# Optimization experiments

Hardware: AMD Instinct MI355X
Metric: run time of the kernel (lower is better)

Reference implementation:

```python
import jax, jax.numpy as jnp
import numpy as np

N_ROWS = 100000   # sparse matrix rows (nodes)
N_COLS = 8192     # input feature dim
UNITS = 128
NNZ = 2000000     # ~20 nonzeros per row


def setup_inputs() -> dict:
    key = jax.random.key(0)
    k1, k2, k3, k4, k5 = jax.random.split(key, 5)
    vals = jax.random.normal(k1, (NNZ,), dtype=jnp.float32)
    rows = jax.random.randint(k2, (NNZ,), 0, N_ROWS, dtype=jnp.int32)
    cols = jax.random.randint(k3, (NNZ,), 0, N_COLS, dtype=jnp.int32)
    # GlorotUniform-style scale for W, matching the TF initializer statistics
    limit = jnp.sqrt(6.0 / (N_COLS + UNITS)).astype(jnp.float32)
    W = jax.random.uniform(k4, (N_COLS, UNITS), dtype=jnp.float32, minval=-limit, maxval=limit)
    b = jax.random.uniform(k5, (UNITS,), dtype=jnp.float32, minval=-limit, maxval=limit)
    return {"vals": vals, "rows": rows, "cols": cols, "W": W, "b": b, "num_rows": N_ROWS}


def reference(vals, rows, cols, W, b, num_rows):
    # sparse (COO) [num_rows, F] @ dense W [F, units]:
    # gather the W row for each nonzero, scale by the nonzero value,
    # then scatter-add into the output row -> segment_sum over `rows`.
    gathered = W[cols] * vals[:, None]            # [nnz, units]
    out = jax.ops.segment_sum(gathered, rows, num_segments=num_rows)  # [num_rows, units]
    return out + b                                 # bias add (use_bias=True)
```

## Files before the change

### kernel.cpp

```cpp
#include <hip/hip_runtime.h>
#include <hip/hip_fp16.h>


#define UNITS 128
#define SCAN_BLK 1024
#define BROW 98
#define CBROW 784
#define NCC 128
#define CCAP 17664
#define CH3 2048
#define SLOTS 40
#define OVF_CAP 256
#define SPILL_CAP 8192


__global__ __launch_bounds__(512, 8) void partition_kernel(
        const float* __restrict__ vals, const int* __restrict__ rows,
        const int* __restrict__ cols, const float* __restrict__ W,
        __half2* __restrict__ Wh, int* __restrict__ ccur,
        float2* __restrict__ sortedA, float2* __restrict__ spill,
        int nnz, int nbcc, int wn2) {
    __shared__ float2 sStage[CH3];
    __shared__ unsigned short sBkt[CH3];
    __shared__ int hist[NCC];
    __shared__ int gdelta[NCC];

    const int t = threadIdx.x;
    const int lane = t & 63;
    const int w = t >> 6;
    const int bb = blockIdx.x;

    {
        const float2* W2 = (const float2*)W;
        int stride = gridDim.x * 512;
        for (int i = bb * 512 + t; i < wn2; i += stride)
            Wh[i] = __float22half2_rn(W2[i]);
    }

    const int chunk0 = bb * CH3;
    int n = nnz - chunk0;
    if (n > CH3) n = CH3;

    if (t < NCC) hist[t] = 0;
    __syncthreads();

    int rbuf[4];
#pragma unroll
    for (int j = 0; j < 4; ++j) {
        int r = j * 512 + t;
        int rv = -1;
        if (r < n) {
            rv = rows[chunk0 + r];
            atomicAdd(&hist[rv / CBROW], 1);
        }
        rbuf[j] = rv;
    }
    __syncthreads();

    if (w == 0) {
        int a0 = hist[2 * lane], a1 = hist[2 * lane + 1];
        int ps = a0 + a1;
        int inc = ps;
#pragma unroll
        for (int o = 1; o < 64; o <<= 1) {
            int u = __shfl_up(inc, o);
            if (lane >= o) inc += u;
        }
        int excl = inc - ps;
        int s0 = 2 * lane, s1 = 2 * lane + 1;
        int g0 = (s0 < nbcc && a0 > 0) ? atomicAdd(&ccur[s0 * 16], a0) : 0;
        int g1 = (s1 < nbcc && a1 > 0) ? atomicAdd(&ccur[s1 * 16], a1) : 0;
        gdelta[s0] = s0 * CCAP + g0 - excl;
        gdelta[s1] = s1 * CCAP + g1 - (excl + a0);
        hist[s0] = excl;
        hist[s1] = excl + a0;
    }
    __syncthreads();

#pragma unroll
    for (int j = 0; j < 4; ++j) {
        int rv = rbuf[j];
        if (rv >= 0) {
            int r = j * 512 + t;
            int bkt = rv / CBROW;
            int rlo = rv - bkt * CBROW;
            int pos = atomicAdd(&hist[bkt], 1);
            float v = vals[chunk0 + r];
            int col = cols[chunk0 + r];
            sStage[pos] = make_float2(v, __int_as_float(col | (rlo << 13)));
            sBkt[pos] = (unsigned short)bkt;
        }
    }
    __syncthreads();

    int* spill_cnt = &ccur[NCC * 16];
    for (int s = t; s < n; s += 512) {
        float2 e = sStage[s];
        int bkt = sBkt[s];
        int dest = gdelta[bkt] + s;
        if (dest < (bkt + 1) * CCAP) {
            sortedA[dest] = e;
        } else {
            int sp = atomicAdd(spill_cnt, 1);
            if (sp < SPILL_CAP) {
                int pk = __float_as_int(e.y);
                int row = bkt * CBROW + (pk >> 13);
                spill[sp] = make_float2(e.x, __int_as_float((pk & 8191) | (row << 13)));
            }
        }
    }
}


__global__ __launch_bounds__(512, 8) void fused_sort_compute_kernel(
        const float2* __restrict__ A, const int* __restrict__ ccur,
        const __half2* __restrict__ Wh, const float* __restrict__ b,
        float* __restrict__ out, const float2* __restrict__ spill, int NR) {
    __shared__ float2 st[BROW * SLOTS];
    __shared__ float2 ovf[OVF_CAP];
    __shared__ int cnt_s[BROW + 6];
    __shared__ int ovf_n;
    __shared__ int spill_n;
    const int t = threadIdx.x;
    const int lane = t & 63;
    const int w = t >> 6;

    const int nwg = gridDim.x;
    const int orig = blockIdx.x;
    const int q = nwg >> 3, r8 = nwg & 7, xcd = orig & 7, idx = orig >> 3;
    const int f = (xcd < r8 ? xcd * (q + 1) : r8 * (q + 1) + (xcd - r8) * q) + idx;

    const int c = f >> 3, sb = f & 7;
    const int r0 = f * BROW;
    const int rlo0 = sb * BROW;
    const size_t base = (size_t)c * CCAP;
    int segn = ccur[c * 16];
    if (segn > CCAP) segn = CCAP;

    const float2 bias = ((const float2*)b)[lane];

    if (t < BROW + 6) cnt_s[t] = 0;
    if (t == 0) {
        ovf_n = 0;
        int sn = ccur[NCC * 16];
        spill_n = (sn > SPILL_CAP) ? SPILL_CAP : sn;
    }
    for (int i = t; i < BROW * SLOTS; i += 512)
        st[i] = make_float2(0.f, __int_as_float(0));
    __syncthreads();

    const float4* A4 = (const float4*)(A + base);
    const int seg2 = segn >> 1;
    for (int k2 = t; k2 < seg2; k2 += 512) {
        float4 qv = A4[k2];
        {
            int pk = __float_as_int(qv.y);
            unsigned rl = (unsigned)(pk >> 13) - rlo0;
            if (rl < BROW) {
                int p = atomicAdd(&cnt_s[rl], 1);
                if (p < SLOTS) st[rl * SLOTS + p] = make_float2(qv.x, __int_as_float(pk & 8191));
                else {
                    int qn = atomicAdd(&ovf_n, 1);
                    if (qn < OVF_CAP) ovf[qn] = make_float2(qv.x, __int_as_float((pk & 8191) | (rl << 13)));
                }
            }
        }
        {
            int pk = __float_as_int(qv.w);
            unsigned rl = (unsigned)(pk >> 13) - rlo0;
            if (rl < BROW) {
                int p = atomicAdd(&cnt_s[rl], 1);
                if (p < SLOTS) st[rl * SLOTS + p] = make_float2(qv.z, __int_as_float(pk & 8191));
                else {
                    int qn = atomicAdd(&ovf_n, 1);
                    if (qn < OVF_CAP) ovf[qn] = make_float2(qv.z, __int_as_float((pk & 8191) | (rl << 13)));
                }
            }
        }
    }
    if ((segn & 1) && t == 0) {
        float2 e = A[base + segn - 1];
        int pk = __float_as_int(e.y);
        unsigned rl = (unsigned)(pk >> 13) - rlo0;
        if (rl < BROW) {
            int p = atomicAdd(&cnt_s[rl], 1);
            if (p < SLOTS) st[rl * SLOTS + p] = make_float2(e.x, __int_as_float(pk & 8191));
            else {
                int qn = atomicAdd(&ovf_n, 1);
                if (qn < OVF_CAP) ovf[qn] = make_float2(e.x, __int_as_float((pk & 8191) | (rl << 13)));
            }
        }
    }
    __syncthreads();

    const int on = (ovf_n > OVF_CAP) ? OVF_CAP : ovf_n;
    const int sn = spill_n;
    for (int rA = w; rA < BROW; rA += 16) {
        const int rB = rA + 8;
        const bool hasB = (rB < BROW);
        int cA = cnt_s[rA]; if (cA > SLOTS) cA = SLOTS; cA = (cA + 3) & ~3;
        int cB = 0;
        if (hasB) { cB = cnt_s[rB]; if (cB > SLOTS) cB = SLOTS; cB = (cB + 3) & ~3; }
        const float2* sA = &st[rA * SLOTS];
        const float2* sB = &st[(hasB ? rB : rA) * SLOTS];
        const int m = (cA > cB) ? cA : cB;
        float axA0 = 0.f, ayA0 = 0.f, axA1 = 0.f, ayA1 = 0.f;
        float axB0 = 0.f, ayB0 = 0.f, axB1 = 0.f, ayB1 = 0.f;
        for (int k = 0; k < m; k += 4) {
            if (k < cA) {
                float2 p0 = sA[k], p1 = sA[k + 1], p2 = sA[k + 2], p3 = sA[k + 3];
                int c0 = __float_as_int(p0.y) & 8191;
                int c1 = __float_as_int(p1.y) & 8191;
                int c2 = __float_as_int(p2.y) & 8191;
                int c3 = __float_as_int(p3.y) & 8191;
                float2 w0 = __half22float2(Wh[c0 * 64 + lane]);
                float2 w1 = __half22float2(Wh[c1 * 64 + lane]);
                float2 w2 = __half22float2(Wh[c2 * 64 + lane]);
                float2 w3 = __half22float2(Wh[c3 * 64 + lane]);
                axA0 += p0.x * w0.x; ayA0 += p0.x * w0.y;
                axA1 += p1.x * w1.x; ayA1 += p1.x * w1.y;
                axA0 += p2.x * w2.x; ayA0 += p2.x * w2.y;
                axA1 += p3.x * w3.x; ayA1 += p3.x * w3.y;
            }
            if (k < cB) {
                float2 p0 = sB[k], p1 = sB[k + 1], p2 = sB[k + 2], p3 = sB[k + 3];
                int c0 = __float_as_int(p0.y) & 8191;
                int c1 = __float_as_int(p1.y) & 8191;
                int c2 = __float_as_int(p2.y) & 8191;
                int c3 = __float_as_int(p3.y) & 8191;
                float2 w0 = __half22float2(Wh[c0 * 64 + lane]);
                float2 w1 = __half22float2(Wh[c1 * 64 + lane]);
                float2 w2 = __half22float2(Wh[c2 * 64 + lane]);
                float2 w3 = __half22float2(Wh[c3 * 64 + lane]);
                axB0 += p0.x * w0.x; ayB0 += p0.x * w0.y;
                axB1 += p1.x * w1.x; ayB1 += p1.x * w1.y;
                axB0 += p2.x * w2.x; ayB0 += p2.x * w2.y;
                axB1 += p3.x * w3.x; ayB1 += p3.x * w3.y;
            }
        }
        {
            int grow = r0 + rA;
            if (grow < NR) {
                for (int q2 = 0; q2 < on; ++q2) {
                    float2 eo = ovf[q2];
                    int pk = __float_as_int(eo.y);
                    if ((pk >> 13) == rA) {
                        float2 wv = __half22float2(Wh[(pk & 8191) * 64 + lane]);
                        axA0 += eo.x * wv.x; ayA0 += eo.x * wv.y;
                    }
                }
                for (int s2 = 0; s2 < sn; ++s2) {
                    float2 es = spill[s2];
                    int pk = __float_as_int(es.y);
                    if ((pk >> 13) == grow) {
                        float2 wv = __half22float2(Wh[(pk & 8191) * 64 + lane]);
                        axA0 += es.x * wv.x; ayA0 += es.x * wv.y;
                    }
                }
                ((float2*)out)[(size_t)grow * 64 + lane] =
                    make_float2(axA0 + axA1 + bias.x, ayA0 + ayA1 + bias.y);
            }
        }
        if (hasB) {
            int grow = r0 + rB;
            if (grow < NR) {
                for (int q2 = 0; q2 < on; ++q2) {
                    float2 eo = ovf[q2];
                    int pk = __float_as_int(eo.y);
                    if ((pk >> 13) == rB) {
                        float2 wv = __half22float2(Wh[(pk & 8191) * 64 + lane]);
                        axB0 += eo.x * wv.x; ayB0 += eo.x * wv.y;
                    }
                }
                for (int s2 = 0; s2 < sn; ++s2) {
                    float2 es = spill[s2];
                    int pk = __float_as_int(es.y);
                    if ((pk >> 13) == grow) {
                        float2 wv = __half22float2(Wh[(pk & 8191) * 64 + lane]);
                        axB0 += es.x * wv.x; ayB0 += es.x * wv.y;
                    }
                }
                ((float2*)out)[(size_t)grow * 64 + lane] =
                    make_float2(axB0 + axB1 + bias.x, ayB0 + ayB1 + bias.y);
            }
        }
    }
}


__global__ void hist_kernel(const int* __restrict__ rows, int* __restrict__ counts, int nnz) {
    int i = blockIdx.x * blockDim.x + threadIdx.x;
    if (i < nnz) atomicAdd(&counts[rows[i]], 1);
}

__global__ void scan1_kernel(const int* __restrict__ counts, int* __restrict__ tmp,
                             int* __restrict__ bsums, int NR, int NS) {
    __shared__ int s[SCAN_BLK];
    int t = threadIdx.x;
    int i = blockIdx.x * SCAN_BLK + t;
    int x = (i < NR) ? counts[i] : 0;
    s[t] = x;
    __syncthreads();
    for (int off = 1; off < SCAN_BLK; off <<= 1) {
        int v = (t >= off) ? s[t - off] : 0;
        __syncthreads();
        s[t] += v;
        __syncthreads();
    }
    if (i < NS) tmp[i] = s[t] - x;
    if (t == SCAN_BLK - 1) bsums[blockIdx.x] = s[SCAN_BLK - 1];
}

__global__ void scan2_kernel(int* __restrict__ bsums, int nb) {
    if (threadIdx.x == 0 && blockIdx.x == 0) {
        int run = 0;
        for (int i = 0; i < nb; ++i) { int c = bsums[i]; bsums[i] = run; run += c; }
    }
}

__global__ void scan3_kernel(const int* __restrict__ tmp, const int* __restrict__ bsums,
                             int* __restrict__ row_start, int* __restrict__ cursor,
                             int NR, int NS) {
    int i = blockIdx.x * blockDim.x + threadIdx.x;
    if (i < NS) {
        int v = tmp[i] + bsums[i >> 10];
        row_start[i] = v;
        if (i < NR) cursor[i] = v;
    }
}

__global__ void scatter_sort_kernel(const float* __restrict__ vals, const int* __restrict__ rows,
                                    const int* __restrict__ cols, int* __restrict__ cursor,
                                    float2* __restrict__ sorted, int nnz) {
    int i = blockIdx.x * blockDim.x + threadIdx.x;
    if (i < nnz) {
        int r = rows[i];
        int p = atomicAdd(&cursor[r], 1);
        sorted[p] = make_float2(vals[i], __int_as_float(cols[i]));
    }
}

__global__ void compute_kernel(const float2* __restrict__ sorted, const int* __restrict__ row_start,
                               const float* __restrict__ W, const float* __restrict__ b,
                               float* __restrict__ out, int NR) {
    int lane = threadIdx.x & 63;
    int wv = threadIdx.x >> 6;
    int row = blockIdx.x * 4 + wv;
    if (row >= NR) return;
    int start = row_start[row];
    int end   = row_start[row + 1];
    const float2* W2 = (const float2*)W;
    float accx0 = 0.f, accy0 = 0.f, accx1 = 0.f, accy1 = 0.f;
    for (int base = start; base < end; base += 64) {
        int m = end - base;
        if (m > 64) m = 64;
        float2 p = make_float2(0.f, __int_as_float(0));
        if (lane < m) p = sorted[base + lane];
        int vi = __float_as_int(p.x);
        int ci = __float_as_int(p.y);
        int rounds = (m + 3) & ~3;
        for (int j = 0; j < rounds; j += 4) {
            float v0 = __int_as_float(__builtin_amdgcn_readlane(vi, j));
            int   c0 = __builtin_amdgcn_readlane(ci, j);
            float v1 = __int_as_float(__builtin_amdgcn_readlane(vi, j + 1));
            int   c1 = __builtin_amdgcn_readlane(ci, j + 1);
            float v2 = __int_as_float(__builtin_amdgcn_readlane(vi, j + 2));
            int   c2 = __builtin_amdgcn_readlane(ci, j + 2);
            float v3 = __int_as_float(__builtin_amdgcn_readlane(vi, j + 3));
            int   c3 = __builtin_amdgcn_readlane(ci, j + 3);
            float2 w0 = W2[c0 * 64 + lane];
            float2 w1 = W2[c1 * 64 + lane];
            float2 w2 = W2[c2 * 64 + lane];
            float2 w3 = W2[c3 * 64 + lane];
            accx0 += v0 * w0.x; accy0 += v0 * w0.y;
            accx1 += v1 * w1.x; accy1 += v1 * w1.y;
            accx0 += v2 * w2.x; accy0 += v2 * w2.y;
            accx1 += v3 * w3.x; accy1 += v3 * w3.y;
        }
    }
    float2 bb = ((const float2*)b)[lane];
    ((float2*)out)[(size_t)row * 64 + lane] =
        make_float2(accx0 + accx1 + bb.x, accy0 + accy1 + bb.y);
}


__global__ void init_bias_kernel(float* __restrict__ out, const float* __restrict__ b, int total4) {
    const float4* b4 = (const float4*)b;
    float4* out4 = (float4*)out;
    int stride = gridDim.x * blockDim.x;
    for (int j = blockIdx.x * blockDim.x + threadIdx.x; j < total4; j += stride)
        out4[j] = b4[j & 31];
}

__global__ void scatter_atomic_kernel(const float* __restrict__ vals, const int* __restrict__ rows,
                                      const int* __restrict__ cols, const float* __restrict__ W,
                                      float* __restrict__ out, int nnz) {
    long long idx = (long long)blockIdx.x * blockDim.x + threadIdx.x;
    int i = (int)(idx >> 5);
    int c = (int)(idx & 31);
    if (i >= nnz) return;
    int row = rows[i], col = cols[i];
    float v = vals[i];
    float4 w = ((const float4*)W)[col * 32 + c];
    float* o = out + (size_t)row * UNITS + (c << 2);
    atomicAdd(o + 0, v * w.x);
    atomicAdd(o + 1, v * w.y);
    atomicAdd(o + 2, v * w.z);
    atomicAdd(o + 3, v * w.w);
}

extern "C" void kernel_launch(void* const* d_in, const int* in_sizes, int n_in,
                              void* d_out, int out_size, void* d_ws, size_t ws_size,
                              hipStream_t stream) {
    const float* vals = (const float*)d_in[0];
    const int*   rows = (const int*)d_in[1];
    const int*   cols = (const int*)d_in[2];
    const float* W    = (const float*)d_in[3];
    const float* b    = (const float*)d_in[4];
    float* out = (float*)d_out;

    const int nnz = in_sizes[0];
    const int NW  = in_sizes[3];
    const int NR  = out_size / UNITS;
    const int NS  = NR + 1;
    const int NB  = (NS + SCAN_BLK - 1) / SCAN_BLK;
    const int nbf  = (NR + BROW - 1) / BROW;
    const int nbcc = (NR + CBROW - 1) / CBROW;

    auto align = [](size_t x) { return (x + 255) & ~(size_t)255; };

    size_t off_ccur    = 0;
    size_t off_wh      = align(off_ccur + (size_t)(NCC * 16 + 1) * 4);
    size_t off_sortedA = align(off_wh + (size_t)NW * 2);
    size_t off_spill   = align(off_sortedA + (size_t)NCC * CCAP * 8);
    size_t needed_full = off_spill + (size_t)SPILL_CAP * 8;

    size_t t2_counts   = 0;
    size_t t2_tmp      = align(t2_counts + (size_t)NR * 4);
    size_t t2_bsums    = align(t2_tmp    + (size_t)NS * 4);
    size_t t2_rowstart = align(t2_bsums  + (size_t)NB * 4);
    size_t t2_cursor   = align(t2_rowstart + (size_t)NS * 4);
    size_t t2_sorted   = align(t2_cursor + (size_t)NR * 4);
    size_t needed_r2   = t2_sorted + (size_t)nnz * 8;

    char* ws = (char*)d_ws;

    if (ws_size >= needed_full && nbcc >= 1 && nbcc <= NCC && NR >= 1) {
        int*     ccur    = (int*)(ws + off_ccur);
        __half2* Wh      = (__half2*)(ws + off_wh);
        float2*  sortedA = (float2*)(ws + off_sortedA);
        float2*  spill   = (float2*)(ws + off_spill);

        hipMemsetAsync(ccur, 0, (size_t)(NCC * 16 + 1) * 4, stream);
        {
            int grid = (nnz + CH3 - 1) / CH3;
            partition_kernel<<<grid, 512, 0, stream>>>(vals, rows, cols, W, Wh,
                                                       ccur, sortedA, spill,
                                                       nnz, nbcc, NW / 2);
        }
        fused_sort_compute_kernel<<<nbf, 512, 0, stream>>>(sortedA, ccur, Wh, b,
                                                           out, spill, NR);
    } else if (ws_size >= needed_r2) {
        int*    counts    = (int*)(ws + t2_counts);
        int*    tmp       = (int*)(ws + t2_tmp);
        int*    bsums     = (int*)(ws + t2_bsums);
        int*    row_start = (int*)(ws + t2_rowstart);
        int*    cursor    = (int*)(ws + t2_cursor);
        float2* sorted    = (float2*)(ws + t2_sorted);

        hipMemsetAsync(counts, 0, (size_t)NR * 4, stream);
        {
            int block = 256, grid = (nnz + block - 1) / block;
            hist_kernel<<<grid, block, 0, stream>>>(rows, counts, nnz);
        }
        scan1_kernel<<<NB, SCAN_BLK, 0, stream>>>(counts, tmp, bsums, NR, NS);
        scan2_kernel<<<1, 64, 0, stream>>>(bsums, NB);
        {
            int block = 256, grid = (NS + block - 1) / block;
            scan3_kernel<<<grid, block, 0, stream>>>(tmp, bsums, row_start, cursor, NR, NS);
        }
        {
            int block = 256, grid = (nnz + block - 1) / block;
            scatter_sort_kernel<<<grid, block, 0, stream>>>(vals, rows, cols, cursor, sorted, nnz);
        }
        {
            int grid = (NR + 3) / 4;
            compute_kernel<<<grid, 256, 0, stream>>>(sorted, row_start, W, b, out, NR);
        }
    } else {
        int total4 = out_size / 4;
        int block = 256;
        int grid = (total4 + block - 1) / block;
        init_bias_kernel<<<grid, block, 0, stream>>>(out, b, total4);
        long long total_threads = (long long)nnz * 32;
        long long g2 = (total_threads + block - 1) / block;
        scatter_atomic_kernel<<<(int)g2, block, 0, stream>>>(vals, rows, cols, W, out, nnz);
    }
}
```

Baseline: 169.8 us.

## Double partition chunk size and make the gather-accumulate loop branchless

Each partition block now handles 4096 nonzeros instead of 2048. The bucket index array shrinks to bytes so LDS use grows less, and the per-thread row buffer doubles. This means fewer blocks, fewer global cursor atomics and fewer scattered writes. In the compute kernel, the two rows processed by a wave are now loaded and accumulated together without per-row branches, padded to the larger of the two counts. This trades extra, possibly wasted, slot reads for more independent W gathers in flight. It relies on unused slots holding zero values and raises LDS use per partition block, which may lower occupancy.

```diff
diff --git a/kernel.cpp b/kernel.cpp
--- a/kernel.cpp
+++ b/kernel.cpp
@@ -8,7 +8,7 @@
 #define CBROW 784
 #define NCC 128
 #define CCAP 17664
-#define CH3 2048
+#define CH3 4096
 #define SLOTS 40
 #define OVF_CAP 256
 #define SPILL_CAP 8192
@@ -21,7 +21,7 @@
         float2* __restrict__ sortedA, float2* __restrict__ spill,
         int nnz, int nbcc, int wn2) {
     __shared__ float2 sStage[CH3];
-    __shared__ unsigned short sBkt[CH3];
+    __shared__ unsigned char sBkt[CH3];
     __shared__ int hist[NCC];
     __shared__ int gdelta[NCC];
 
@@ -44,9 +44,9 @@
     if (t < NCC) hist[t] = 0;
     __syncthreads();
 
-    int rbuf[4];
+    int rbuf[8];
 #pragma unroll
-    for (int j = 0; j < 4; ++j) {
+    for (int j = 0; j < 8; ++j) {
         int r = j * 512 + t;
         int rv = -1;
         if (r < n) {
@@ -78,7 +78,7 @@
     __syncthreads();
 
 #pragma unroll
-    for (int j = 0; j < 4; ++j) {
+    for (int j = 0; j < 8; ++j) {
         int rv = rbuf[j];
         if (rv >= 0) {
             int r = j * 512 + t;
@@ -88,7 +88,7 @@
             float v = vals[chunk0 + r];
             int col = cols[chunk0 + r];
             sStage[pos] = make_float2(v, __int_as_float(col | (rlo << 13)));
-            sBkt[pos] = (unsigned short)bkt;
+            sBkt[pos] = (unsigned char)bkt;
         }
     }
     __syncthreads();
@@ -198,45 +198,42 @@
     for (int rA = w; rA < BROW; rA += 16) {
         const int rB = rA + 8;
         const bool hasB = (rB < BROW);
-        int cA = cnt_s[rA]; if (cA > SLOTS) cA = SLOTS; cA = (cA + 3) & ~3;
+        int cA = cnt_s[rA]; if (cA > SLOTS) cA = SLOTS;
         int cB = 0;
-        if (hasB) { cB = cnt_s[rB]; if (cB > SLOTS) cB = SLOTS; cB = (cB + 3) & ~3; }
+        if (hasB) { cB = cnt_s[rB]; if (cB > SLOTS) cB = SLOTS; }
         const float2* sA = &st[rA * SLOTS];
         const float2* sB = &st[(hasB ? rB : rA) * SLOTS];
-        const int m = (cA > cB) ? cA : cB;
+        int m = (cA > cB) ? cA : cB;
+        m = (m + 3) & ~3;
         float axA0 = 0.f, ayA0 = 0.f, axA1 = 0.f, ayA1 = 0.f;
         float axB0 = 0.f, ayB0 = 0.f, axB1 = 0.f, ayB1 = 0.f;
         for (int k = 0; k < m; k += 4) {
-            if (k < cA) {
-                float2 p0 = sA[k], p1 = sA[k + 1], p2 = sA[k + 2], p3 = sA[k + 3];
-                int c0 = __float_as_int(p0.y) & 8191;
-                int c1 = __float_as_int(p1.y) & 8191;
-                int c2 = __float_as_int(p2.y) & 8191;
-                int c3 = __float_as_int(p3.y) & 8191;
-                float2 w0 = __half22float2(Wh[c0 * 64 + lane]);
-                float2 w1 = __half22float2(Wh[c1 * 64 + lane]);
-                float2 w2 = __half22float2(Wh[c2 * 64 + lane]);
-                float2 w3 = __half22float2(Wh[c3 * 64 + lane]);
-                axA0 += p0.x * w0.x; ayA0 += p0.x * w0.y;
-                axA1 += p1.x * w1.x; ayA1 += p1.x * w1.y;
-                axA0 += p2.x * w2.x; ayA0 += p2.x * w2.y;
-                axA1 += p3.x * w3.x; ayA1 += p3.x * w3.y;
-            }
-            if (k < cB) {
-                float2 p0 = sB[k], p1 = sB[k + 1], p2 = sB[k + 2], p3 = sB[k + 3];
-                int c0 = __float_as_int(p0.y) & 8191;
-                int c1 = __float_as_int(p1.y) & 8191;
-                int c2 = __float_as_int(p2.y) & 8191;
-                int c3 = __float_as_int(p3.y) & 8191;
-                float2 w0 = __half22float2(Wh[c0 * 64 + lane]);
-                float2 w1 = __half22float2(Wh[c1 * 64 + lane]);
-                float2 w2 = __half22float2(Wh[c2 * 64 + lane]);
-                float2 w3 = __half22float2(Wh[c3 * 64 + lane]);
-                axB0 += p0.x * w0.x; ayB0 += p0.x * w0.y;
-                axB1 += p1.x * w1.x; ayB1 += p1.x * w1.y;
-                axB0 += p2.x * w2.x; ayB0 += p2.x * w2.y;
-                axB1 += p3.x * w3.x; ayB1 += p3.x * w3.y;
-            }
+            float2 a0 = sA[k], a1 = sA[k + 1], a2 = sA[k + 2], a3 = sA[k + 3];
+            float2 b0 = sB[k], b1 = sB[k + 1], b2 = sB[k + 2], b3 = sB[k + 3];
+            int ca0 = __float_as_int(a0.y) & 8191;
+            int ca1 = __float_as_int(a1.y) & 8191;
+            int ca2 = __float_as_int(a2.y) & 8191;
+            int ca3 = __float_as_int(a3.y) & 8191;
+            int cb0 = __float_as_int(b0.y) & 8191;
+            int cb1 = __float_as_int(b1.y) & 8191;
+            int cb2 = __float_as_int(b2.y) & 8191;
+            int cb3 = __float_as_int(b3.y) & 8191;
+            float2 wa0 = __half22float2(Wh[ca0 * 64 + lane]);
+            float2 wa1 = __half22float2(Wh[ca1 * 64 + lane]);
+            float2 wa2 = __half22float2(Wh[ca2 * 64 + lane]);
+            float2 wa3 = __half22float2(Wh[ca3 * 64 + lane]);
+            float2 wb0 = __half22float2(Wh[cb0 * 64 + lane]);
+            float2 wb1 = __half22float2(Wh[cb1 * 64 + lane]);
+            float2 wb2 = __half22float2(Wh[cb2 * 64 + lane]);
+            float2 wb3 = __half22float2(Wh[cb3 * 64 + lane]);
+            axA0 += a0.x * wa0.x; ayA0 += a0.x * wa0.y;
+            axA1 += a1.x * wa1.x; ayA1 += a1.x * wa1.y;
+            axA0 += a2.x * wa2.x; ayA0 += a2.x * wa2.y;
+            axA1 += a3.x * wa3.x; ayA1 += a3.x * wa3.y;
+            axB0 += b0.x * wb0.x; ayB0 += b0.x * wb0.y;
+            axB1 += b1.x * wb1.x; ayB1 += b1.x * wb1.y;
+            axB0 += b2.x * wb2.x; ayB0 += b2.x * wb2.y;
+            axB1 += b3.x * wb3.x; ayB1 += b3.x * wb3.y;
         }
         {
             int grow = r0 + rA;
```

Result: faster. 156.5 us (-7.8%).
